# Performance work log

Hardware: AMD Instinct MI355X
Metric: run time of the kernel (lower is better)

The kernel has to match this reference:

```python
import jax, jax.numpy as jnp
import numpy as np

# Hop node counts (targets of layer i are sources of layer i+1) and sampling fanouts
N = [1081344, 67584, 6144, 1024]
FANOUT = [15, 10, 5]
D = 128  # in_channels == hidden_channels


def setup_inputs() -> dict:
    key = jax.random.key(0)
    ks = jax.random.split(key, 10)
    inp = {"x": jax.random.normal(ks[0], (N[0], D), dtype=jnp.float32)}
    for i in range(3):
        Ns, Nt, f = N[i], N[i + 1], FANOUT[i]
        inp[f"src{i}"] = jax.random.randint(ks[1 + i], (Nt * f,), 0, Ns, dtype=jnp.int32)
        # each target node has exactly `fanout` sampled neighbors
        inp[f"dst{i}"] = jnp.repeat(jnp.arange(Nt, dtype=jnp.int32), f)
        inp[f"W_l{i}"] = jax.random.normal(ks[4 + i], (D, D), dtype=jnp.float32) * 0.1
        inp[f"W_r{i}"] = jax.random.normal(ks[7 + i], (D, D), dtype=jnp.float32) * 0.1
    return inp


def _sage_conv(x, src, dst, n_target, W_l, W_r):
    # mean-aggregate source features into targets (PyG SAGEConv, aggr='mean', bias=False)
    msg = jax.ops.segment_sum(x[src], dst, num_segments=n_target)          # [Nt, D]
    deg = jax.ops.segment_sum(jnp.ones(src.shape, x.dtype), dst, num_segments=n_target)
    mean = msg / jnp.maximum(deg, 1.0)[:, None]
    return mean @ W_l.T + x[:n_target] @ W_r.T


def reference(x, W_l0, W_r0, W_l1, W_r1, W_l2, W_r2,
              src0, dst0, src1, dst1, src2, dst2):
    Wl = [W_l0, W_l1, W_l2]
    Wr = [W_r0, W_r1, W_r2]
    srcs = [src0, src1, src2]
    dsts = [dst0, dst1, dst2]
    for i in range(3):
        x = _sage_conv(x, srcs[i], dsts[i], N[i + 1], Wl[i], Wr[i])
        if i != 2:
            x = jax.nn.relu(x)  # dropout omitted (eval mode / p acts as identity here)
    return jax.nn.log_softmax(x, axis=-1)
```

## Files before the change

### kernel.cpp

```cpp
#include <hip/hip_runtime.h>

#define D 128

__global__ void build_wt_all(const float* __restrict__ Wl0, const float* __restrict__ Wr0,
                             const float* __restrict__ Wl1, const float* __restrict__ Wr1,
                             const float* __restrict__ Wl2, const float* __restrict__ Wr2,
                             float* __restrict__ WT ) {
    const int layer = blockIdx.x >> 7;
    const int i = (blockIdx.x & 127) * 256 + threadIdx.x;
    const float* Wl = (layer == 0) ? Wl0 : (layer == 1) ? Wl1 : Wl2;
    const float* Wr = (layer == 0) ? Wr0 : (layer == 1) ? Wr1 : Wr2;
    const int k = i >> 7;
    const int d = i & 127;
    const float v = (k < D) ? Wl[d * D + k] : Wr[d * D + (k - D)];
    WT[layer * 2 * D * D + i] = v;
}

template <int F>
__global__ __launch_bounds__(256, 4) void sage_layer(
        const float* __restrict__ x,
        const int*   __restrict__ src,
        const float* __restrict__ WT,
        float*       __restrict__ out,
        int doRelu) {
    constexpr int M = 32;
    __shared__ float A[M][2 * D];

    const int tid  = threadIdx.x;
    const int lane = tid & 63;
    const int wave = tid >> 6;
    const int t0   = blockIdx.x * M;

    const float2* __restrict__ x2 = (const float2*)x;
    const float inv = 1.0f / (float)F;
    for (int mi = wave; mi < M; mi += 4) {
        const int t = t0 + mi;
        const int base = t * F;
        float2 acc = make_float2(0.f, 0.f);
#pragma unroll
        for (int j = 0; j < F; ++j) {
            const int s = src[base + j];
            const float2 v = x2[(size_t)s * 64 + lane];
            acc.x += v.x;
            acc.y += v.y;
        }
        const float2 xt = x2[(size_t)t * 64 + lane];
        A[mi][2 * lane]         = acc.x * inv;
        A[mi][2 * lane + 1]     = acc.y * inv;
        A[mi][D + 2 * lane]     = xt.x;
        A[mi][D + 2 * lane + 1] = xt.y;
    }
    __syncthreads();

    const int d = tid & (D - 1);
    const int r = tid >> 7;
    float acc[M / 2];
#pragma unroll
    for (int m = 0; m < M / 2; ++m) acc[m] = 0.f;

#pragma unroll 2
    for (int k = 0; k < 2 * D; k += 4) {
        const float w0 = WT[(k + 0) * D + d];
        const float w1 = WT[(k + 1) * D + d];
        const float w2 = WT[(k + 2) * D + d];
        const float w3 = WT[(k + 3) * D + d];
#pragma unroll
        for (int m = 0; m < M / 2; ++m) {
            const float4 a = *(const float4*)&A[2 * m + r][k];
            acc[m] = fmaf(a.x, w0, acc[m]);
            acc[m] = fmaf(a.y, w1, acc[m]);
            acc[m] = fmaf(a.z, w2, acc[m]);
            acc[m] = fmaf(a.w, w3, acc[m]);
        }
    }

#pragma unroll
    for (int m = 0; m < M / 2; ++m) {
        const int row = t0 + 2 * m + r;
        float v = acc[m];
        if (doRelu) v = fmaxf(v, 0.f);
        out[(size_t)row * D + d] = v;
    }
}

__global__ void log_softmax_k(float* __restrict__ io, int Nrows) {
    const int lane = threadIdx.x & 63;
    const int wave = threadIdx.x >> 6;
    const int row  = blockIdx.x * 4 + wave;
    if (row >= Nrows) return;
    float2* p = (float2*)(io + (size_t)row * D);
    const float2 v = p[lane];

    float m = fmaxf(v.x, v.y);
#pragma unroll
    for (int o = 32; o; o >>= 1) m = fmaxf(m, __shfl_xor(m, o, 64));

    float e = __expf(v.x - m) + __expf(v.y - m);
#pragma unroll
    for (int o = 32; o; o >>= 1) e += __shfl_xor(e, o, 64);

    const float ls = __logf(e) + m;
    p[lane] = make_float2(v.x - ls, v.y - ls);
}

extern "C" void kernel_launch(void* const* d_in, const int* in_sizes, int n_in,
                              void* d_out, int out_size, void* d_ws, size_t ws_size,
                              hipStream_t stream) {
    const float* x   = (const float*)d_in[0];
    const int*   src0 = (const int*)d_in[1];
    const float* Wl0 = (const float*)d_in[3];
    const float* Wr0 = (const float*)d_in[4];
    const int*   src1 = (const int*)d_in[5];
    const float* Wl1 = (const float*)d_in[7];
    const float* Wr1 = (const float*)d_in[8];
    const int*   src2 = (const int*)d_in[9];
    const float* Wl2 = (const float*)d_in[11];
    const float* Wr2 = (const float*)d_in[12];

    float* ws  = (float*)d_ws;
    float* WT0 = ws;
    float* WT1 = ws + 32768;
    float* WT2 = ws + 65536;
    float* h0  = ws + 98304;
    float* h1  = h0 + 67584 * 128;
    float* outF = (float*)d_out;

    build_wt_all<<<384, 256, 0, stream>>>(Wl0, Wr0, Wl1, Wr1, Wl2, Wr2, WT0);

    sage_layer<15><<<67584 / 32, 256, 0, stream>>>(x,  src0, WT0, h0,  1);
    sage_layer<10><<<6144  / 32, 256, 0, stream>>>(h0, src1, WT1, h1,  1);
    sage_layer<5> <<<1024  / 32, 256, 0, stream>>>(h1, src2, WT2, outF, 0);

    log_softmax_k<<<1024 / 4, 256, 0, stream>>>(outF, 1024);
}
```

Measured before the change: 907.4 us.

## Use bf16 MFMA for SAGE layer GEMMs with bf16 intermediates and fused log-softmax

The per-layer dense projection now runs on bf16 MFMA 16x16x32 instructions instead of scalar FP32 FMAs. Weights are pre-transposed into bf16, and the aggregated and self features are staged in shared memory as bf16. Hidden activations h0 and h1 are stored as bf16, which halves gather traffic in the later layers. Log-softmax is fused into the last layer's epilogue, and the block tile grows to 64 rows. The trade-off is reduced precision in the features and weights, which risks tolerance failures.

Result: faster. 777.3 us (-14.3%).

```diff
diff --git a/kernel.cpp b/kernel.cpp
--- a/kernel.cpp
+++ b/kernel.cpp
@@ -1,135 +1,161 @@
 #include <hip/hip_runtime.h>
+#include <stdint.h>
 
 #define D 128
 
-__global__ void build_wt_all(const float* __restrict__ Wl0, const float* __restrict__ Wr0,
-                             const float* __restrict__ Wl1, const float* __restrict__ Wr1,
-                             const float* __restrict__ Wl2, const float* __restrict__ Wr2,
-                             float* __restrict__ WT ) {
+typedef __attribute__((ext_vector_type(8))) short frag8;
+typedef __attribute__((ext_vector_type(4))) float fragc;
+
+__device__ __forceinline__ short f2bf(float f) {
+    uint32_t u = __float_as_uint(f);
+    u += 0x7fffu + ((u >> 16) & 1u);
+    return (short)(u >> 16);
+}
+__device__ __forceinline__ float bf2f(unsigned short h) {
+    return __uint_as_float(((uint32_t)h) << 16);
+}
+
+__global__ void build_wtt(const float* __restrict__ Wl0, const float* __restrict__ Wr0,
+                          const float* __restrict__ Wl1, const float* __restrict__ Wr1,
+                          const float* __restrict__ Wl2, const float* __restrict__ Wr2,
+                          short* __restrict__ WTt) {
     const int layer = blockIdx.x >> 7;
     const int i = (blockIdx.x & 127) * 256 + threadIdx.x;
     const float* Wl = (layer == 0) ? Wl0 : (layer == 1) ? Wl1 : Wl2;
     const float* Wr = (layer == 0) ? Wr0 : (layer == 1) ? Wr1 : Wr2;
-    const int k = i >> 7;
-    const int d = i & 127;
+    const int d = i >> 8;
+    const int k = i & 255;
     const float v = (k < D) ? Wl[d * D + k] : Wr[d * D + (k - D)];
-    WT[layer * 2 * D * D + i] = v;
+    WTt[layer * 32768 + i] = f2bf(v);
 }
 
-template <int F>
-__global__ __launch_bounds__(256, 4) void sage_layer(
-        const float* __restrict__ x,
-        const int*   __restrict__ src,
-        const float* __restrict__ WT,
-        float*       __restrict__ out,
-        int doRelu) {
-    constexpr int M = 32;
-    __shared__ float A[M][2 * D];
+template <int F, typename TIN, typename TOUT, bool RELU, bool SOFTMAX>
+__global__ __launch_bounds__(256, 4) void sage_mfma(
+        const TIN* __restrict__ x,
+        const int* __restrict__ src,
+        const short* __restrict__ WTt,
+        TOUT* __restrict__ out) {
+    constexpr int M = 64;
+    constexpr int AS = 264;
+    __shared__ short A[M * AS];
 
     const int tid  = threadIdx.x;
     const int lane = tid & 63;
     const int wave = tid >> 6;
     const int t0   = blockIdx.x * M;
 
-    const float2* __restrict__ x2 = (const float2*)x;
     const float inv = 1.0f / (float)F;
     for (int mi = wave; mi < M; mi += 4) {
         const int t = t0 + mi;
-        const int base = t * F;
-        float2 acc = make_float2(0.f, 0.f);
+        const long base = (long)t * F;
+        float ax = 0.f, ay = 0.f;
 #pragma unroll
         for (int j = 0; j < F; ++j) {
             const int s = src[base + j];
-            const float2 v = x2[(size_t)s * 64 + lane];
-            acc.x += v.x;
-            acc.y += v.y;
+            if constexpr (sizeof(TIN) == 4) {
+                const float2 v = ((const float2*)x)[(size_t)s * 64 + lane];
+                ax += v.x; ay += v.y;
+            } else {
+                const ushort2 u = ((const ushort2*)x)[(size_t)s * 64 + lane];
+                ax += bf2f(u.x); ay += bf2f(u.y);
+            }
         }
-        const float2 xt = x2[(size_t)t * 64 + lane];
-        A[mi][2 * lane]         = acc.x * inv;
-        A[mi][2 * lane + 1]     = acc.y * inv;
-        A[mi][D + 2 * lane]     = xt.x;
-        A[mi][D + 2 * lane + 1] = xt.y;
+        short sx, sy;
+        if constexpr (sizeof(TIN) == 4) {
+            const float2 v = ((const float2*)x)[(size_t)t * 64 + lane];
+            sx = f2bf(v.x); sy = f2bf(v.y);
+        } else {
+            const ushort2 u = ((const ushort2*)x)[(size_t)t * 64 + lane];
+            sx = (short)u.x; sy = (short)u.y;
+        }
+        *(short2*)&A[mi * AS + 2 * lane]     = make_short2(f2bf(ax * inv), f2bf(ay * inv));
+        *(short2*)&A[mi * AS + D + 2 * lane] = make_short2(sx, sy);
     }
     __syncthreads();
 
-    const int d = tid & (D - 1);
-    const int r = tid >> 7;
-    float acc[M / 2];
+    const int m    = lane & 15;
+    const int quad = lane >> 4;
+    const int r0   = wave * 16;
+
+    frag8 af[8];
+    const short* arow = &A[(r0 + m) * AS + quad * 8];
 #pragma unroll
-    for (int m = 0; m < M / 2; ++m) acc[m] = 0.f;
+    for (int ks = 0; ks < 8; ++ks)
+        af[ks] = *(const frag8*)(arow + ks * 32);
 
-#pragma unroll 2
-    for (int k = 0; k < 2 * D; k += 4) {
-        const float w0 = WT[(k + 0) * D + d];
-        const float w1 = WT[(k + 1) * D + d];
-        const float w2 = WT[(k + 2) * D + d];
-        const float w3 = WT[(k + 3) * D + d];
+    fragc acc[8];
 #pragma unroll
-        for (int m = 0; m < M / 2; ++m) {
-            const float4 a = *(const float4*)&A[2 * m + r][k];
-            acc[m] = fmaf(a.x, w0, acc[m]);
-            acc[m] = fmaf(a.y, w1, acc[m]);
-            acc[m] = fmaf(a.z, w2, acc[m]);
-            acc[m] = fmaf(a.w, w3, acc[m]);
+    for (int ct = 0; ct < 8; ++ct) acc[ct] = (fragc)0.f;
+
+#pragma unroll
+    for (int ks = 0; ks < 8; ++ks) {
+        const short* bbase = WTt + m * 256 + ks * 32 + quad * 8;
+#pragma unroll
+        for (int ct = 0; ct < 8; ++ct) {
+            const frag8 bf = *(const frag8*)(bbase + ct * 16 * 256);
+            acc[ct] = __builtin_amdgcn_mfma_f32_16x16x32_bf16(af[ks], bf, acc[ct], 0, 0, 0);
         }
     }
 
+    if constexpr (!SOFTMAX) {
 #pragma unroll
-    for (int m = 0; m < M / 2; ++m) {
-        const int row = t0 + 2 * m + r;
-        float v = acc[m];
-        if (doRelu) v = fmaxf(v, 0.f);
-        out[(size_t)row * D + d] = v;
+        for (int ct = 0; ct < 8; ++ct) {
+#pragma unroll
+            for (int reg = 0; reg < 4; ++reg) {
+                float v = acc[ct][reg];
+                if constexpr (RELU) v = fmaxf(v, 0.f);
+                const int row = t0 + r0 + quad * 4 + reg;
+                const int col = ct * 16 + m;
+                if constexpr (sizeof(TOUT) == 2)
+                    out[(size_t)row * D + col] = (TOUT)f2bf(v);
+                else
+                    out[(size_t)row * D + col] = (TOUT)v;
+            }
+        }
+    } else {
+#pragma unroll
+        for (int reg = 0; reg < 4; ++reg) {
+            float mx = -3.4e38f;
+#pragma unroll
+            for (int ct = 0; ct < 8; ++ct) mx = fmaxf(mx, acc[ct][reg]);
+#pragma unroll
+            for (int off = 1; off < 16; off <<= 1) mx = fmaxf(mx, __shfl_xor(mx, off, 64));
+            float s = 0.f;
+#pragma unroll
+            for (int ct = 0; ct < 8; ++ct) s += __expf(acc[ct][reg] - mx);
+#pragma unroll
+            for (int off = 1; off < 16; off <<= 1) s += __shfl_xor(s, off, 64);
+            const float ls = __logf(s) + mx;
+            const int row = t0 + r0 + quad * 4 + reg;
+#pragma unroll
+            for (int ct = 0; ct < 8; ++ct)
+                ((float*)out)[(size_t)row * D + ct * 16 + m] = acc[ct][reg] - ls;
+        }
     }
-}
-
-__global__ void log_softmax_k(float* __restrict__ io, int Nrows) {
-    const int lane = threadIdx.x & 63;
-    const int wave = threadIdx.x >> 6;
-    const int row  = blockIdx.x * 4 + wave;
-    if (row >= Nrows) return;
-    float2* p = (float2*)(io + (size_t)row * D);
-    const float2 v = p[lane];
-
-    float m = fmaxf(v.x, v.y);
-#pragma unroll
-    for (int o = 32; o; o >>= 1) m = fmaxf(m, __shfl_xor(m, o, 64));
-
-    float e = __expf(v.x - m) + __expf(v.y - m);
-#pragma unroll
-    for (int o = 32; o; o >>= 1) e += __shfl_xor(e, o, 64);
-
-    const float ls = __logf(e) + m;
-    p[lane] = make_float2(v.x - ls, v.y - ls);
 }
 
 extern "C" void kernel_launch(void* const* d_in, const int* in_sizes, int n_in,
                               void* d_out, int out_size, void* d_ws, size_t ws_size,
                               hipStream_t stream) {
-    const float* x   = (const float*)d_in[0];
+    const float* x    = (const float*)d_in[0];
     const int*   src0 = (const int*)d_in[1];
-    const float* Wl0 = (const float*)d_in[3];
-    const float* Wr0 = (const float*)d_in[4];
+    const float* Wl0  = (const float*)d_in[3];
+    const float* Wr0  = (const float*)d_in[4];
     const int*   src1 = (const int*)d_in[5];
-    const float* Wl1 = (const float*)d_in[7];
-    const float* Wr1 = (const float*)d_in[8];
+    const float* Wl1  = (const float*)d_in[7];
+    const float* Wr1  = (const float*)d_in[8];
     const int*   src2 = (const int*)d_in[9];
-    const float* Wl2 = (const float*)d_in[11];
-    const float* Wr2 = (const float*)d_in[12];
+    const float* Wl2  = (const float*)d_in[11];
+    const float* Wr2  = (const float*)d_in[12];
 
-    float* ws  = (float*)d_ws;
-    float* WT0 = ws;
-    float* WT1 = ws + 32768;
-    float* WT2 = ws + 65536;
-    float* h0  = ws + 98304;
-    float* h1  = h0 + 67584 * 128;
+    short* WTt = (short*)d_ws;
+    short* h0  = WTt + 3 * 32768;
+    short* h1  = h0 + 67584 * 128;
     float* outF = (float*)d_out;
 
-    build_wt_all<<<384, 256, 0, stream>>>(Wl0, Wr0, Wl1, Wr1, Wl2, Wr2, WT0);
+    build_wtt<<<384, 256, 0, stream>>>(Wl0, Wr0, Wl1, Wr1, Wl2, Wr2, WTt);
 
-    sage_layer<15><<<67584 / 32, 256, 0, stream>>>(x,  src0, WT0, h0,  1);
-    sage_layer<10><<<6144  / 32, 256, 0, stream>>>(h0, src1, WT1, h1,  1);
-    sage_layer<5> <<<1024  / 32, 256, 0, stream>>>(h1, src2, WT2, outF, 0);
-
-    log_softmax_k<<<1024 / 4, 256, 0, stream>>>(outF, 1024);
+    sage_mfma<15, float, short, true,  false><<<67584 / 64, 256, 0, stream>>>(x,  src0, WTt,          h0);
+    sage_mfma<10, short, short, true,  false><<<6144  / 64, 256, 0, stream>>>(h0, src1, WTt + 32768,  h1);
+    sage_mfma<5,  short, float, false, true ><<<1024  / 64, 256, 0, stream>>>(h1, src2, WTt + 65536,  outF);
 }
```
